# Performance work log

Measured on AMD Instinct MI355X. Metric: run time of the kernel, lower is better.

## Reference

```python
import jax, jax.numpy as jnp
import numpy as np

N, H, W, DIM = 16, 64, 64, 256
HEADS, ANCH = 8, 8
HD = DIM // HEADS  # 32


def setup_inputs() -> dict:
    key = jax.random.key(0)
    ks = jax.random.split(key, 5)
    s = 0.02
    return {
        "x": jax.random.normal(ks[0], (N, H, W, DIM), jnp.float32),
        "W_proj": jax.random.normal(ks[1], (2 * DIM, DIM), jnp.float32) * s,
        "b_proj": jax.random.normal(ks[2], (2 * DIM,), jnp.float32) * s,
        "W_out": jax.random.normal(ks[3], (DIM, DIM), jnp.float32) * s,
        "b_out": jax.random.normal(ks[4], (DIM,), jnp.float32) * s,
        "alpha": jnp.ones((1,), jnp.float32),
        "beta": jnp.zeros((1,), jnp.float32),
    }


def _l2norm(v, axis):
    # matches torch F.normalize(dim=axis, eps=1e-12)
    return v / jnp.maximum(jnp.linalg.norm(v, axis=axis, keepdims=True), 1e-12)


def reference(x, W_proj, b_proj, W_out, b_out, alpha, beta):
    n, h, w, dim = x.shape
    heads, a = HEADS, ANCH
    hd = dim // heads
    m = n * heads
    # proj -> (n,h,w,2*dim) -> (n,2*dim,h,w) -> (m, 2*hd, h, w)
    xp = (x @ W_proj.T + b_proj).transpose(0, 3, 1, 2).reshape(m, 2 * hd, h, w)
    flat = xp.reshape(m, 2 * hd, h * w)
    point0, value0 = flat[:, :hd], flat[:, hd:]          # (m, hd, hw) each
    # adaptive max pool to (a,a); h,w divisible by a so uniform windows
    pooled = xp.reshape(m, 2 * hd, a, h // a, a, w // a).max(axis=(3, 5))
    pooled = pooled.reshape(m, 2 * hd, a * a)
    point1, value1 = pooled[:, :hd], pooled[:, hd:]      # (m, hd, a2) each
    point0, point1 = _l2norm(point0, 1), _l2norm(point1, 1)
    # cosine similarity: (m, hw, a2)
    sim = jnp.einsum('mdp,mda->mpa', point0, point1)
    sim = jax.nn.sigmoid(alpha[0] * sim + beta[0])
    # hard top-1 routing over anchors
    idx = jnp.argmax(sim, axis=-1)                       # (m, hw)
    sim = jax.nn.one_hot(idx, a * a, dtype=sim.dtype) * sim  # (m, hw, a2)
    # aggregate values into anchors: sum_p value0[m,d,p]*sim[m,p,a] + value1
    agg = jnp.einsum('mdp,mpa->mda', value0, sim) + value1   # (m, hd, a2)
    agg = agg / (sim.sum(axis=1)[:, None, :] + 1.0)
    # broadcast back to points: sum_a sim[m,p,a]*agg[m,d,a]
    msg = jnp.einsum('mpa,mda->mdp', sim, agg)               # (m, hd, hw)
    msg = msg.reshape(n, dim, h, w).transpose(0, 2, 3, 1)    # (n,h,w,dim)
    return msg @ W_out.T + b_out
```

## Files before the change

kernel.cpp:

```cpp
#include <hip/hip_runtime.h>
#include <float.h>
#include <math.h>


#define NPIX   4096
#define NIMG   16
#define TOTPIX 65536
#define DIM2   512

typedef __attribute__((ext_vector_type(8))) short bf16x8;
typedef __attribute__((ext_vector_type(4))) float f32x4;

#define BM 128
#define BN 128
#define BK 32

__global__ __launch_bounds__(512, 2) void proj_point(
    const float* __restrict__ X, const float* __restrict__ W,
    const float* __restrict__ bias, float* __restrict__ XP) {
  __shared__ float As[BK][BM];
  __shared__ float Bs[BK][BN];
  const int tid = threadIdx.x;
  const int M0 = blockIdx.x * BM, C0 = blockIdx.y * BN;
  const int tm = tid >> 5, tn = tid & 31;

  const int r = tid & 127;
  const int kq = (tid >> 7) << 3;

  const int pcr = C0 + r;
  const float* Xa = X + (size_t)(M0 + r) * 256 + kq;
  const float* Wb = W + (size_t)((pcr >> 5) * 64 + (pcr & 31)) * 256 + kq;

  float4 xa0, xa1, wb0, wb1;

#define LOADT(ko)                                                      \
  do {                                                                 \
    xa0 = *(const float4*)(Xa + (ko));                                 \
    xa1 = *(const float4*)(Xa + (ko) + 4);                             \
    wb0 = *(const float4*)(Wb + (ko));                                 \
    wb1 = *(const float4*)(Wb + (ko) + 4);                             \
  } while (0)

  float acc[8][4];
#pragma unroll
  for (int i = 0; i < 8; ++i)
#pragma unroll
    for (int j = 0; j < 4; ++j) acc[i][j] = 0.f;

  LOADT(0);

  for (int k0 = 0; k0 < 256; k0 += BK) {
    __syncthreads();
#pragma unroll
    for (int j = 0; j < 4; ++j) {
      As[kq + j][r]     = (&xa0.x)[j];
      As[kq + 4 + j][r] = (&xa1.x)[j];
      Bs[kq + j][r]     = (&wb0.x)[j];
      Bs[kq + 4 + j][r] = (&wb1.x)[j];
    }
    __syncthreads();
    if (k0 + BK < 256) LOADT(k0 + BK);
#pragma unroll
    for (int kk = 0; kk < BK; ++kk) {
      float a[8], b[4];
      *(float4*)&a[0] = *(const float4*)&As[kk][tm * 8];
      *(float4*)&a[4] = *(const float4*)&As[kk][tm * 8 + 4];
      *(float4*)&b[0] = *(const float4*)&Bs[kk][tn * 4];
#pragma unroll
      for (int i = 0; i < 8; ++i)
#pragma unroll
        for (int j = 0; j < 4; ++j)
          acc[i][j] = fmaf(a[i], b[j], acc[i][j]);
    }
  }

  const int c = C0 + tn * 4;
  const int pcol = (c >> 5) * 64 + (c & 31);
  const float4 bq = *(const float4*)(bias + pcol);
#pragma unroll
  for (int i = 0; i < 8; ++i) {
    const size_t row = (size_t)(M0 + tm * 8 + i) * DIM2 + pcol;
    float4 o;
    o.x = acc[i][0] + bq.x; o.y = acc[i][1] + bq.y;
    o.z = acc[i][2] + bq.z; o.w = acc[i][3] + bq.w;
    *(float4*)(XP + row) = o;
  }
}

__device__ __forceinline__ void split2(float x, unsigned short& h1,
                                       unsigned short& h2) {
  unsigned u1 = __float_as_uint(x);
  h1 = (unsigned short)(u1 >> 16);
  float r1 = x - __uint_as_float(u1 & 0xFFFF0000u);
  h2 = (unsigned short)(__float_as_uint(r1) >> 16);
}

__global__ __launch_bounds__(256, 2) void proj_value(
    const float* __restrict__ X, const float* __restrict__ W,
    const float* __restrict__ bias, float* __restrict__ XP) {
  __shared__ unsigned char lds[4 * 8192];
  const int tid = threadIdx.x;
  const int M0 = blockIdx.x * 128;
  const int V0 = blockIdx.y * 128;

  const int w = tid >> 6, l = tid & 63;
  const int wm = w >> 1, wn = w & 1;

  const int jj = tid & 7;
  const int rsub = tid >> 3;

  const float* Xbase = X + (size_t)M0 * 256;

  float4 ra[4], rb[4];
#define GLOADV(kofs)                                                          \
  do {                                                                        \
    _Pragma("unroll") for (int i = 0; i < 4; ++i) {                           \
      ra[i] = *(const float4*)(Xbase + (size_t)(i * 32 + rsub) * 256 + (kofs) + jj * 4); \
      rb[i] = *(const float4*)(W + (size_t)((((V0 >> 5) + i) * 64) + 32 + rsub) * 256 + (kofs) + jj * 4); \
    }                                                                         \
  } while (0)

  f32x4 acc[4][4] = {};

  const int fr = l & 15, kg = l >> 4;
  const int chunk = kg << 4;

  GLOADV(0);

  for (int s = 0; s < 8; ++s) {
    __syncthreads();
#pragma unroll
    for (int i = 0; i < 4; ++i) {
      const int row = i * 32 + rsub;
      const int off = row * 64 + jj * 8;
      unsigned short a1[4], a2[4], b1[4], b2[4];
#pragma unroll
      for (int e = 0; e < 4; ++e) {
        split2(((const float*)&ra[i])[e], a1[e], a2[e]);
        split2(((const float*)&rb[i])[e], b1[e], b2[e]);
      }
#define PK2(arr) make_uint2((unsigned)(arr)[0] | ((unsigned)(arr)[1] << 16),  \
                            (unsigned)(arr)[2] | ((unsigned)(arr)[3] << 16))
      *(uint2*)(lds + 0 * 8192 + off) = PK2(a1);
      *(uint2*)(lds + 1 * 8192 + off) = PK2(a2);
      *(uint2*)(lds + 2 * 8192 + off) = PK2(b1);
      *(uint2*)(lds + 3 * 8192 + off) = PK2(b2);
#undef PK2
    }
    __syncthreads();
    if (s < 7) GLOADV((s + 1) * 32);

    bf16x8 af[4][2];
#pragma unroll
    for (int mi = 0; mi < 4; ++mi) {
      const int base = (wm * 64 + mi * 16 + fr) * 64 + chunk;
      af[mi][0] = *(const bf16x8*)(lds + 0 * 8192 + base);
      af[mi][1] = *(const bf16x8*)(lds + 1 * 8192 + base);
    }
#pragma unroll
    for (int ni = 0; ni < 4; ++ni) {
      const int base = (wn * 64 + ni * 16 + fr) * 64 + chunk;
      const bf16x8 b1 = *(const bf16x8*)(lds + 2 * 8192 + base);
      const bf16x8 b2 = *(const bf16x8*)(lds + 3 * 8192 + base);
#pragma unroll
      for (int mi = 0; mi < 4; ++mi) {
        f32x4 c = acc[mi][ni];
        c = __builtin_amdgcn_mfma_f32_16x16x32_bf16(af[mi][0], b1, c, 0, 0, 0);
        c = __builtin_amdgcn_mfma_f32_16x16x32_bf16(af[mi][0], b2, c, 0, 0, 0);
        c = __builtin_amdgcn_mfma_f32_16x16x32_bf16(af[mi][1], b1, c, 0, 0, 0);
        acc[mi][ni] = c;
      }
    }
  }

  const int orow0 = M0 + wm * 64 + (l >> 4) * 4;
#pragma unroll
  for (int ni = 0; ni < 4; ++ni) {
    const int vc = V0 + wn * 64 + ni * 16 + fr;
    const int pcol = (vc >> 5) * 64 + 32 + (vc & 31);
    const float bv = bias[pcol];
#pragma unroll
    for (int mi = 0; mi < 4; ++mi)
#pragma unroll
      for (int j = 0; j < 4; ++j)
        XP[(size_t)(orow0 + mi * 16 + j) * DIM2 + pcol] = acc[mi][ni][j] + bv;
  }
}

__global__ __launch_bounds__(256) void pool_norm(
    const float* __restrict__ XP, float* __restrict__ P1N,
    float* __restrict__ V1) {
  const int n = blockIdx.x, a = blockIdx.y;
  const int ay = a >> 3, ax = a & 7;
  const int tid = threadIdx.x;
  const size_t base = ((size_t)n * NPIX + (size_t)(ay * 8) * 64 + ax * 8) * DIM2;
  const int c0 = tid * 2;
  float m0 = -FLT_MAX, m1 = -FLT_MAX;
#pragma unroll
  for (int iy = 0; iy < 8; ++iy) {
    const float* rowp = XP + base + (size_t)iy * 64 * DIM2;
#pragma unroll
    for (int ix = 0; ix < 8; ++ix) {
      const float2 v = *(const float2*)(rowp + (size_t)ix * DIM2 + c0);
      m0 = fmaxf(m0, v.x);
      m1 = fmaxf(m1, v.y);
    }
  }
  const int m = n * 8 + (tid >> 5);
  const int l32 = tid & 31;
  float s0 = m0 * m0, s1 = m1 * m1;
#pragma unroll
  for (int o = 8; o > 0; o >>= 1) {
    s0 += __shfl_xor(s0, o, 32);
    s1 += __shfl_xor(s1, o, 32);
  }
  const float sq = s0 + s1;
  if (l32 < 16) {
    const float rn = 1.0f / fmaxf(sqrtf(sq), 1e-12f);
    float2 o2; o2.x = m0 * rn; o2.y = m1 * rn;
    *(float2*)(P1N + ((size_t)m * 64 + a) * 32 + 2 * l32) = o2;
  } else {
    float2 o2; o2.x = m0; o2.y = m1;
    *(float2*)(V1 + ((size_t)m * 64 + a) * 32 + 2 * (l32 - 16)) = o2;
  }
}

__global__ __launch_bounds__(256) void sim_argmax(
    const float* __restrict__ XP, const float* __restrict__ P1N,
    const float* __restrict__ alpha, const float* __restrict__ beta,
    float* __restrict__ SV, int* __restrict__ IDX) {
  const int m = blockIdx.x, chunk = blockIdx.y;
  const int n = m >> 3, h = m & 7;
  __shared__ float P1[64][32];
  const int tid = threadIdx.x;
  {
    const float4* src = (const float4*)(P1N + (size_t)m * 2048);
    float4* dst = (float4*)&P1[0][0];
    dst[tid] = src[tid];
    dst[tid + 256] = src[tid + 256];
  }
  __syncthreads();
  const float al = alpha[0], be = beta[0];

  const int p0 = chunk * 256 + tid;
  const int p1 = p0 + 2048;
  const float* row0 = XP + ((size_t)n * NPIX + p0) * DIM2 + h * 64;
  const float* row1 = XP + ((size_t)n * NPIX + p1) * DIM2 + h * 64;

  float v0[32], v1[32];
#pragma unroll
  for (int q = 0; q < 8; ++q) {
    float4 t0 = ((const float4*)row0)[q];
    float4 t1 = ((const float4*)row1)[q];
    v0[q * 4 + 0] = t0.x; v0[q * 4 + 1] = t0.y; v0[q * 4 + 2] = t0.z; v0[q * 4 + 3] = t0.w;
    v1[q * 4 + 0] = t1.x; v1[q * 4 + 1] = t1.y; v1[q * 4 + 2] = t1.z; v1[q * 4 + 3] = t1.w;
  }
  float ss0 = 0.f, ss1 = 0.f;
#pragma unroll
  for (int d = 0; d < 32; ++d) { ss0 += v0[d] * v0[d]; ss1 += v1[d] * v1[d]; }
  const float rn0 = 1.0f / fmaxf(sqrtf(ss0), 1e-12f);
  const float rn1 = 1.0f / fmaxf(sqrtf(ss1), 1e-12f);
#pragma unroll
  for (int d = 0; d < 32; ++d) { v0[d] *= rn0; v1[d] *= rn1; }

  float best0 = -1.f, best1 = -1.f;
  int bi0 = 0, bi1 = 0;
  for (int a = 0; a < 64; ++a) {
    float d0a = 0.f, d0b = 0.f, d1a = 0.f, d1b = 0.f;
#pragma unroll
    for (int d = 0; d < 16; ++d) {
      const float wa = P1[a][2 * d], wb = P1[a][2 * d + 1];
      d0a = fmaf(v0[2 * d], wa, d0a);
      d0b = fmaf(v0[2 * d + 1], wb, d0b);
      d1a = fmaf(v1[2 * d], wa, d1a);
      d1b = fmaf(v1[2 * d + 1], wb, d1b);
    }
    const float t0 = al * (d0a + d0b) + be;
    const float t1 = al * (d1a + d1b) + be;
    const float s0 = 1.0f / (1.0f + expf(-t0));
    const float s1 = 1.0f / (1.0f + expf(-t1));
    if (s0 > best0) { best0 = s0; bi0 = a; }
    if (s1 > best1) { best1 = s1; bi1 = a; }
  }
  SV[(size_t)m * NPIX + p0] = best0;
  IDX[(size_t)m * NPIX + p0] = bi0;
  SV[(size_t)m * NPIX + p1] = best1;
  IDX[(size_t)m * NPIX + p1] = bi1;
}

#define NSEG 4
__global__ __launch_bounds__(256) void scatter_partial(
    const float* __restrict__ XP, const float* __restrict__ SV,
    const int* __restrict__ IDX, float* __restrict__ PART) {
  const int m = blockIdx.x, seg = blockIdx.y;
  const int n = m >> 3, h = m & 7;
  __shared__ float agg[8][32][65];
  __shared__ float ssum[8][64];
  const int tid = threadIdx.x;
  const int g = tid >> 5, d = tid & 31;

  for (int e = tid; e < 8 * 32 * 65; e += 256) ((float*)agg)[e] = 0.f;
  for (int e = tid; e < 8 * 64; e += 256) ((float*)ssum)[e] = 0.f;
  __syncthreads();

  const size_t svbase = (size_t)m * NPIX;
  const int pbase = seg * 1024 + g * 128;
  int lastid = -1;
  float acc = 0.f, accS = 0.f;
  for (int i0 = 0; i0 < 128; i0 += 4) {
    const int p = pbase + i0;
    const float4 sv4 = *(const float4*)(SV + svbase + p);
    const int4 id4 = *(const int4*)(IDX + svbase + p);
    float vv4[4];
#pragma unroll
    for (int j = 0; j < 4; ++j)
      vv4[j] = XP[((size_t)n * NPIX + p + j) * DIM2 + h * 64 + 32 + d];
#pragma unroll
    for (int j = 0; j < 4; ++j) {
      const float sv = (&sv4.x)[j];
      const int id = (&id4.x)[j];
      if (id != lastid) {
        if (lastid >= 0) {
          agg[g][d][lastid] += acc;
          if (d == 0) ssum[g][lastid] += accS;
        }
        lastid = id; acc = 0.f; accS = 0.f;
      }
      acc = fmaf(vv4[j], sv, acc);
      accS += sv;
    }
  }
  if (lastid >= 0) {
    agg[g][d][lastid] += acc;
    if (d == 0) ssum[g][lastid] += accS;
  }
  __syncthreads();

  float* P = PART + (size_t)(m * NSEG + seg) * 2112;
  for (int e = tid; e < 2048; e += 256) {
    const int dd = e >> 6, aa = e & 63;
    float s = 0.f;
#pragma unroll
    for (int gg = 0; gg < 8; ++gg) s += agg[gg][dd][aa];
    P[e] = s;
  }
  if (tid < 64) {
    float s = 0.f;
#pragma unroll
    for (int gg = 0; gg < 8; ++gg) s += ssum[gg][tid];
    P[2048 + tid] = s;
  }
}

__global__ __launch_bounds__(256) void reduce_proj(
    const float* __restrict__ PART, const float* __restrict__ V1,
    const float* __restrict__ Wout, float* __restrict__ PA) {
  const int m = blockIdx.x;
  const int h = m & 7;
  __shared__ float aggF[64][33];
  __shared__ float ssumF[64];
  const int tid = threadIdx.x;
  const float* P = PART + (size_t)m * NSEG * 2112;

  if (tid < 64) {
    float s = 0.f;
#pragma unroll
    for (int seg = 0; seg < NSEG; ++seg) s += P[seg * 2112 + 2048 + tid];
    ssumF[tid] = s + 1.0f;
  }
  __syncthreads();

  for (int e = tid; e < 2048; e += 256) {
    const int dd = e >> 6, aa = e & 63;
    float s = 0.f;
#pragma unroll
    for (int seg = 0; seg < NSEG; ++seg) s += P[seg * 2112 + e];
    s += V1[((size_t)m * 64 + aa) * 32 + dd];
    aggF[aa][dd] = s / ssumF[aa];
  }
  __syncthreads();

  float w[32];
  const float* wrow = Wout + (size_t)tid * 256 + h * 32;
#pragma unroll
  for (int q = 0; q < 8; ++q) {
    const float4 t = ((const float4*)wrow)[q];
    w[q * 4 + 0] = t.x; w[q * 4 + 1] = t.y; w[q * 4 + 2] = t.z; w[q * 4 + 3] = t.w;
  }
  for (int aa = 0; aa < 64; ++aa) {
    float s0 = 0.f, s1 = 0.f;
#pragma unroll
    for (int d2 = 0; d2 < 16; ++d2) {
      s0 = fmaf(w[2 * d2], aggF[aa][2 * d2], s0);
      s1 = fmaf(w[2 * d2 + 1], aggF[aa][2 * d2 + 1], s1);
    }
    PA[((size_t)m * 64 + aa) * 256 + tid] = s0 + s1;
  }
}

__global__ __launch_bounds__(256) void out_assemble(
    const float* __restrict__ PA, const float* __restrict__ SV,
    const int* __restrict__ IDX, const float* __restrict__ bout,
    float* __restrict__ OUT) {
  const int tid = threadIdx.x;
  const int lp = tid >> 6, lane = tid & 63;
  const size_t p = (size_t)blockIdx.x * 4 + lp;
  const int n = (int)(p >> 12);
  const int pp = (int)(p & 4095);
  float4 acc = ((const float4*)bout)[lane];
#pragma unroll
  for (int h = 0; h < 8; ++h) {
    const int m = n * 8 + h;
    const float sv = SV[(size_t)m * NPIX + pp];
    const int id = IDX[(size_t)m * NPIX + pp];
    const float4 pa = ((const float4*)(PA + ((size_t)m * 64 + id) * 256))[lane];
    acc.x = fmaf(sv, pa.x, acc.x);
    acc.y = fmaf(sv, pa.y, acc.y);
    acc.z = fmaf(sv, pa.z, acc.z);
    acc.w = fmaf(sv, pa.w, acc.w);
  }
  ((float4*)OUT)[p * 64 + lane] = acc;
}

extern "C" void kernel_launch(void* const* d_in, const int* in_sizes, int n_in,
                              void* d_out, int out_size, void* d_ws, size_t ws_size,
                              hipStream_t stream) {
  const float* x     = (const float*)d_in[0];
  const float* Wp    = (const float*)d_in[1];
  const float* bp    = (const float*)d_in[2];
  const float* Wo    = (const float*)d_in[3];
  const float* bo    = (const float*)d_in[4];
  const float* alpha = (const float*)d_in[5];
  const float* beta  = (const float*)d_in[6];
  float* out = (float*)d_out;

  char* ws = (char*)d_ws;
  float* XP   = (float*)(ws);
  float* P1N  = (float*)(ws + 134217728u);
  float* V1   = (float*)(ws + 135266304u);
  float* SVv  = (float*)(ws + 136314880u);
  int*   IDX  = (int*)  (ws + 138412032u);
  float* PA   = (float*)(ws + 140509184u);
  float* PART = (float*)(ws + 148897792u);
  (void)in_sizes; (void)n_in; (void)out_size; (void)ws_size;

  proj_point     <<<dim3(512, 2), 512, 0, stream>>>(x, Wp, bp, XP);
  proj_value     <<<dim3(512, 2), 256, 0, stream>>>(x, Wp, bp, XP);
  pool_norm      <<<dim3(16, 64), 256, 0, stream>>>(XP, P1N, V1);
  sim_argmax     <<<dim3(128, 8), 256, 0, stream>>>(XP, P1N, alpha, beta, SVv, IDX);
  scatter_partial<<<dim3(128, NSEG), 256, 0, stream>>>(XP, SVv, IDX, PART);
  reduce_proj    <<<128, 256, 0, stream>>>(PART, V1, Wo, PA);
  out_assemble   <<<16384, 256, 0, stream>>>(PA, SVv, IDX, bo, out);
}
```

Before: 323.3 us.

## Fuse point and value projection kernels into one interleaved launch

Merges the FP32 point-projection GEMM and the split-bf16 MFMA value-projection GEMM into a single 2048-block launch. Even and odd blocks take the two paths, so FMA-bound and MFMA-bound work can share CUs at the same time and one launch boundary goes away. The value path is resized to 512 threads, with 8 waves each covering a 64x32 sub-tile. The cost is a bigger register footprint for the fused kernel, which may lower occupancy, and divergent block roles.

After: 361.9 us. 11.9% more time.

```diff
diff --git a/kernel.cpp b/kernel.cpp
--- a/kernel.cpp
+++ b/kernel.cpp
@@ -14,78 +14,6 @@
 #define BM 128
 #define BN 128
 #define BK 32
-
-__global__ __launch_bounds__(512, 2) void proj_point(
-    const float* __restrict__ X, const float* __restrict__ W,
-    const float* __restrict__ bias, float* __restrict__ XP) {
-  __shared__ float As[BK][BM];
-  __shared__ float Bs[BK][BN];
-  const int tid = threadIdx.x;
-  const int M0 = blockIdx.x * BM, C0 = blockIdx.y * BN;
-  const int tm = tid >> 5, tn = tid & 31;
-
-  const int r = tid & 127;
-  const int kq = (tid >> 7) << 3;
-
-  const int pcr = C0 + r;
-  const float* Xa = X + (size_t)(M0 + r) * 256 + kq;
-  const float* Wb = W + (size_t)((pcr >> 5) * 64 + (pcr & 31)) * 256 + kq;
-
-  float4 xa0, xa1, wb0, wb1;
-
-#define LOADT(ko)                                                      \
-  do {                                                                 \
-    xa0 = *(const float4*)(Xa + (ko));                                 \
-    xa1 = *(const float4*)(Xa + (ko) + 4);                             \
-    wb0 = *(const float4*)(Wb + (ko));                                 \
-    wb1 = *(const float4*)(Wb + (ko) + 4);                             \
-  } while (0)
-
-  float acc[8][4];
-#pragma unroll
-  for (int i = 0; i < 8; ++i)
-#pragma unroll
-    for (int j = 0; j < 4; ++j) acc[i][j] = 0.f;
-
-  LOADT(0);
-
-  for (int k0 = 0; k0 < 256; k0 += BK) {
-    __syncthreads();
-#pragma unroll
-    for (int j = 0; j < 4; ++j) {
-      As[kq + j][r]     = (&xa0.x)[j];
-      As[kq + 4 + j][r] = (&xa1.x)[j];
-      Bs[kq + j][r]     = (&wb0.x)[j];
-      Bs[kq + 4 + j][r] = (&wb1.x)[j];
-    }
-    __syncthreads();
-    if (k0 + BK < 256) LOADT(k0 + BK);
-#pragma unroll
-    for (int kk = 0; kk < BK; ++kk) {
-      float a[8], b[4];
-      *(float4*)&a[0] = *(const float4*)&As[kk][tm * 8];
-      *(float4*)&a[4] = *(const float4*)&As[kk][tm * 8 + 4];
-      *(float4*)&b[0] = *(const float4*)&Bs[kk][tn * 4];
-#pragma unroll
-      for (int i = 0; i < 8; ++i)
-#pragma unroll
-        for (int j = 0; j < 4; ++j)
-          acc[i][j] = fmaf(a[i], b[j], acc[i][j]);
-    }
-  }
-
-  const int c = C0 + tn * 4;
-  const int pcol = (c >> 5) * 64 + (c & 31);
-  const float4 bq = *(const float4*)(bias + pcol);
-#pragma unroll
-  for (int i = 0; i < 8; ++i) {
-    const size_t row = (size_t)(M0 + tm * 8 + i) * DIM2 + pcol;
-    float4 o;
-    o.x = acc[i][0] + bq.x; o.y = acc[i][1] + bq.y;
-    o.z = acc[i][2] + bq.z; o.w = acc[i][3] + bq.w;
-    *(float4*)(XP + row) = o;
-  }
-}
 
 __device__ __forceinline__ void split2(float x, unsigned short& h1,
                                        unsigned short& h2) {
@@ -95,95 +23,173 @@
   h2 = (unsigned short)(__float_as_uint(r1) >> 16);
 }
 
-__global__ __launch_bounds__(256, 2) void proj_value(
+__global__ __launch_bounds__(512, 2) void proj_fused(
     const float* __restrict__ X, const float* __restrict__ W,
     const float* __restrict__ bias, float* __restrict__ XP) {
-  __shared__ unsigned char lds[4 * 8192];
-  const int tid = threadIdx.x;
-  const int M0 = blockIdx.x * 128;
-  const int V0 = blockIdx.y * 128;
-
-  const int w = tid >> 6, l = tid & 63;
-  const int wm = w >> 1, wn = w & 1;
-
-  const int jj = tid & 7;
-  const int rsub = tid >> 3;
-
-  const float* Xbase = X + (size_t)M0 * 256;
-
-  float4 ra[4], rb[4];
+  __shared__ char smem[32768];
+  const int tid = threadIdx.x;
+  const int bid = blockIdx.x;
+
+  if ((bid & 1) == 0) {
+    const int pbid = bid >> 1;
+    const int M0 = (pbid & 511) * BM;
+    const int C0 = (pbid >> 9) * BN;
+    float (*As)[BM] = (float (*)[BM])smem;
+    float (*Bs)[BN] = (float (*)[BN])(smem + 16384);
+    const int tm = tid >> 5, tn = tid & 31;
+
+    const int r = tid & 127;
+    const int kq = (tid >> 7) << 3;
+
+    const int pcr = C0 + r;
+    const float* Xa = X + (size_t)(M0 + r) * 256 + kq;
+    const float* Wb = W + (size_t)((pcr >> 5) * 64 + (pcr & 31)) * 256 + kq;
+
+    float4 xa0, xa1, wb0, wb1;
+
+#define LOADT(ko)                                                      \
+    do {                                                               \
+      xa0 = *(const float4*)(Xa + (ko));                               \
+      xa1 = *(const float4*)(Xa + (ko) + 4);                           \
+      wb0 = *(const float4*)(Wb + (ko));                               \
+      wb1 = *(const float4*)(Wb + (ko) + 4);                           \
+    } while (0)
+
+    float acc[8][4];
+#pragma unroll
+    for (int i = 0; i < 8; ++i)
+#pragma unroll
+      for (int j = 0; j < 4; ++j) acc[i][j] = 0.f;
+
+    LOADT(0);
+
+    for (int k0 = 0; k0 < 256; k0 += BK) {
+      __syncthreads();
+#pragma unroll
+      for (int j = 0; j < 4; ++j) {
+        As[kq + j][r]     = (&xa0.x)[j];
+        As[kq + 4 + j][r] = (&xa1.x)[j];
+        Bs[kq + j][r]     = (&wb0.x)[j];
+        Bs[kq + 4 + j][r] = (&wb1.x)[j];
+      }
+      __syncthreads();
+      if (k0 + BK < 256) LOADT(k0 + BK);
+#pragma unroll
+      for (int kk = 0; kk < BK; ++kk) {
+        float a[8], b[4];
+        *(float4*)&a[0] = *(const float4*)&As[kk][tm * 8];
+        *(float4*)&a[4] = *(const float4*)&As[kk][tm * 8 + 4];
+        *(float4*)&b[0] = *(const float4*)&Bs[kk][tn * 4];
+#pragma unroll
+        for (int i = 0; i < 8; ++i)
+#pragma unroll
+          for (int j = 0; j < 4; ++j)
+            acc[i][j] = fmaf(a[i], b[j], acc[i][j]);
+      }
+    }
+
+    const int c = C0 + tn * 4;
+    const int pcol = (c >> 5) * 64 + (c & 31);
+    const float4 bq = *(const float4*)(bias + pcol);
+#pragma unroll
+    for (int i = 0; i < 8; ++i) {
+      const size_t row = (size_t)(M0 + tm * 8 + i) * DIM2 + pcol;
+      float4 o;
+      o.x = acc[i][0] + bq.x; o.y = acc[i][1] + bq.y;
+      o.z = acc[i][2] + bq.z; o.w = acc[i][3] + bq.w;
+      *(float4*)(XP + row) = o;
+    }
+  } else {
+    const int vbid = bid >> 1;
+    const int M0 = (vbid & 511) * 128;
+    const int V0 = (vbid >> 9) * 128;
+    unsigned char* lds = (unsigned char*)smem;
+
+    const int w = tid >> 6, l = tid & 63;
+    const int wm = w >> 2, wn = w & 3;
+
+    const int jj = tid & 7;
+    const int rsub = tid >> 3;
+
+    const float* Xbase = X + (size_t)M0 * 256;
+
+    float4 ra[2], rb[2];
 #define GLOADV(kofs)                                                          \
-  do {                                                                        \
-    _Pragma("unroll") for (int i = 0; i < 4; ++i) {                           \
-      ra[i] = *(const float4*)(Xbase + (size_t)(i * 32 + rsub) * 256 + (kofs) + jj * 4); \
-      rb[i] = *(const float4*)(W + (size_t)((((V0 >> 5) + i) * 64) + 32 + rsub) * 256 + (kofs) + jj * 4); \
-    }                                                                         \
-  } while (0)
-
-  f32x4 acc[4][4] = {};
-
-  const int fr = l & 15, kg = l >> 4;
-  const int chunk = kg << 4;
-
-  GLOADV(0);
-
-  for (int s = 0; s < 8; ++s) {
-    __syncthreads();
-#pragma unroll
-    for (int i = 0; i < 4; ++i) {
-      const int row = i * 32 + rsub;
-      const int off = row * 64 + jj * 8;
-      unsigned short a1[4], a2[4], b1[4], b2[4];
-#pragma unroll
-      for (int e = 0; e < 4; ++e) {
-        split2(((const float*)&ra[i])[e], a1[e], a2[e]);
-        split2(((const float*)&rb[i])[e], b1[e], b2[e]);
-      }
+    do {                                                                      \
+      _Pragma("unroll") for (int i = 0; i < 2; ++i) {                         \
+        const int row_ = i * 64 + rsub;                                       \
+        ra[i] = *(const float4*)(Xbase + (size_t)row_ * 256 + (kofs) + jj * 4); \
+        const int vcrow_ = V0 + row_;                                         \
+        const int wrow_ = (vcrow_ >> 5) * 64 + 32 + (vcrow_ & 31);            \
+        rb[i] = *(const float4*)(W + (size_t)wrow_ * 256 + (kofs) + jj * 4);  \
+      }                                                                       \
+    } while (0)
+
+    f32x4 acc[4][2] = {};
+
+    const int fr = l & 15, kg = l >> 4;
+    const int chunk = kg << 4;
+
+    GLOADV(0);
+
+    for (int s = 0; s < 8; ++s) {
+      __syncthreads();
+#pragma unroll
+      for (int i = 0; i < 2; ++i) {
+        const int row_ = i * 64 + rsub;
+        const int off = row_ * 64 + jj * 8;
+        unsigned short a1[4], a2[4], b1[4], b2[4];
+#pragma unroll
+        for (int e = 0; e < 4; ++e) {
+          split2(((const float*)&ra[i])[e], a1[e], a2[e]);
+          split2(((const float*)&rb[i])[e], b1[e], b2[e]);
+        }
 #define PK2(arr) make_uint2((unsigned)(arr)[0] | ((unsigned)(arr)[1] << 16),  \
                             (unsigned)(arr)[2] | ((unsigned)(arr)[3] << 16))
-      *(uint2*)(lds + 0 * 8192 + off) = PK2(a1);
-      *(uint2*)(lds + 1 * 8192 + off) = PK2(a2);
-      *(uint2*)(lds + 2 * 8192 + off) = PK2(b1);
-      *(uint2*)(lds + 3 * 8192 + off) = PK2(b2);
+        *(uint2*)(lds + 0 * 8192 + off) = PK2(a1);
+        *(uint2*)(lds + 1 * 8192 + off) = PK2(a2);
+        *(uint2*)(lds + 2 * 8192 + off) = PK2(b1);
+        *(uint2*)(lds + 3 * 8192 + off) = PK2(b2);
 #undef PK2
-    }
-    __syncthreads();
-    if (s < 7) GLOADV((s + 1) * 32);
-
-    bf16x8 af[4][2];
-#pragma unroll
-    for (int mi = 0; mi < 4; ++mi) {
-      const int base = (wm * 64 + mi * 16 + fr) * 64 + chunk;
-      af[mi][0] = *(const bf16x8*)(lds + 0 * 8192 + base);
-      af[mi][1] = *(const bf16x8*)(lds + 1 * 8192 + base);
-    }
-#pragma unroll
-    for (int ni = 0; ni < 4; ++ni) {
-      const int base = (wn * 64 + ni * 16 + fr) * 64 + chunk;
-      const bf16x8 b1 = *(const bf16x8*)(lds + 2 * 8192 + base);
-      const bf16x8 b2 = *(const bf16x8*)(lds + 3 * 8192 + base);
+      }
+      __syncthreads();
+      if (s < 7) GLOADV((s + 1) * 32);
+
+      bf16x8 af[4][2];
 #pragma unroll
       for (int mi = 0; mi < 4; ++mi) {
-        f32x4 c = acc[mi][ni];
-        c = __builtin_amdgcn_mfma_f32_16x16x32_bf16(af[mi][0], b1, c, 0, 0, 0);
-        c = __builtin_amdgcn_mfma_f32_16x16x32_bf16(af[mi][0], b2, c, 0, 0, 0);
-        c = __builtin_amdgcn_mfma_f32_16x16x32_bf16(af[mi][1], b1, c, 0, 0, 0);
-        acc[mi][ni] = c;
-      }
-    }
-  }
-
-  const int orow0 = M0 + wm * 64 + (l >> 4) * 4;
-#pragma unroll
-  for (int ni = 0; ni < 4; ++ni) {
-    const int vc = V0 + wn * 64 + ni * 16 + fr;
-    const int pcol = (vc >> 5) * 64 + 32 + (vc & 31);
-    const float bv = bias[pcol];
-#pragma unroll
-    for (int mi = 0; mi < 4; ++mi)
-#pragma unroll
-      for (int j = 0; j < 4; ++j)
-        XP[(size_t)(orow0 + mi * 16 + j) * DIM2 + pcol] = acc[mi][ni][j] + bv;
+        const int base = (wm * 64 + mi * 16 + fr) * 64 + chunk;
+        af[mi][0] = *(const bf16x8*)(lds + 0 * 8192 + base);
+        af[mi][1] = *(const bf16x8*)(lds + 1 * 8192 + base);
+      }
+#pragma unroll
+      for (int ni = 0; ni < 2; ++ni) {
+        const int base = (wn * 32 + ni * 16 + fr) * 64 + chunk;
+        const bf16x8 b1 = *(const bf16x8*)(lds + 2 * 8192 + base);
+        const bf16x8 b2 = *(const bf16x8*)(lds + 3 * 8192 + base);
+#pragma unroll
+        for (int mi = 0; mi < 4; ++mi) {
+          f32x4 c = acc[mi][ni];
+          c = __builtin_amdgcn_mfma_f32_16x16x32_bf16(af[mi][0], b1, c, 0, 0, 0);
+          c = __builtin_amdgcn_mfma_f32_16x16x32_bf16(af[mi][0], b2, c, 0, 0, 0);
+          c = __builtin_amdgcn_mfma_f32_16x16x32_bf16(af[mi][1], b1, c, 0, 0, 0);
+          acc[mi][ni] = c;
+        }
+      }
+    }
+
+    const int orow0 = M0 + wm * 64 + (l >> 4) * 4;
+#pragma unroll
+    for (int ni = 0; ni < 2; ++ni) {
+      const int vc = V0 + wn * 32 + ni * 16 + fr;
+      const int pcol = (vc >> 5) * 64 + 32 + (vc & 31);
+      const float bv = bias[pcol];
+#pragma unroll
+      for (int mi = 0; mi < 4; ++mi)
+#pragma unroll
+        for (int j = 0; j < 4; ++j)
+          XP[(size_t)(orow0 + mi * 16 + j) * DIM2 + pcol] = acc[mi][ni][j] + bv;
+    }
   }
 }
 
@@ -444,8 +450,7 @@
   float* PART = (float*)(ws + 148897792u);
   (void)in_sizes; (void)n_in; (void)out_size; (void)ws_size;
 
-  proj_point     <<<dim3(512, 2), 512, 0, stream>>>(x, Wp, bp, XP);
-  proj_value     <<<dim3(512, 2), 256, 0, stream>>>(x, Wp, bp, XP);
+  proj_fused     <<<2048, 512, 0, stream>>>(x, Wp, bp, XP);
   pool_norm      <<<dim3(16, 64), 256, 0, stream>>>(XP, P1N, V1);
   sim_argmax     <<<dim3(128, 8), 256, 0, stream>>>(XP, P1N, alpha, beta, SVv, IDX);
   scatter_partial<<<dim3(128, NSEG), 256, 0, stream>>>(XP, SVv, IDX, PART);
```
